# Kernel tuning notes

Measured on AMD Instinct MI355X. Metric: run time of the kernel, lower is better.

The kernel has to match this reference:

```python
import jax, jax.numpy as jnp
import numpy as np

N_NODES = 100000
N_EDGES = 1600000
C = 64            # in_channels == out_channels
EC = 32           # edge_channels


def setup_inputs() -> dict:
    key = jax.random.key(0)
    ks = jax.random.split(key, 8)
    s = 1.0 / np.sqrt(C)
    x = jax.random.normal(ks[0], (N_NODES, C), dtype=jnp.float32)
    edge_index = jax.random.randint(ks[1], (2, N_EDGES), 0, N_NODES, dtype=jnp.int64)
    edge_attr = jax.random.normal(ks[2], (N_EDGES, EC), dtype=jnp.float32)
    We = jax.random.uniform(ks[3], (C, EC), minval=-1/np.sqrt(EC), maxval=1/np.sqrt(EC), dtype=jnp.float32)  # edge_lin weight
    W = jax.random.uniform(ks[4], (C, C), minval=-s, maxval=s, dtype=jnp.float32)   # GatedGraphConv weight[0]
    W_ih = jax.random.uniform(ks[5], (3 * C, C), minval=-s, maxval=s, dtype=jnp.float32)
    W_hh = jax.random.uniform(ks[6], (3 * C, C), minval=-s, maxval=s, dtype=jnp.float32)
    b_ih = jnp.zeros((3 * C,), dtype=jnp.float32)
    b_hh = jnp.zeros((3 * C,), dtype=jnp.float32)
    return {"x": x, "edge_index": edge_index, "edge_attr": edge_attr,
            "We": We, "W": W, "W_ih": W_ih, "W_hh": W_hh, "b_ih": b_ih, "b_hh": b_hh}


def reference(x, edge_index, edge_attr, We, W, W_ih, W_hh, b_ih, b_hh):
    n_nodes = x.shape[0]
    # edge_lin: [E, EC] -> [E, C]
    ew = edge_attr @ We.T
    # GatedGraphConv, num_layers=1, aggr='add'
    m = x @ W                                  # [N, C]
    src, dst = edge_index[0], edge_index[1]
    msg = m[src] * ew                          # gather + elementwise edge weight, [E, C]
    agg = jax.ops.segment_sum(msg, dst, num_segments=n_nodes)  # scatter-add
    # GRUCell(agg, x)
    gi = agg @ W_ih.T + b_ih                   # [N, 3C]
    gh = x @ W_hh.T + b_hh                     # [N, 3C]
    i_r, i_z, i_n = jnp.split(gi, 3, axis=-1)
    h_r, h_z, h_n = jnp.split(gh, 3, axis=-1)
    r = jax.nn.sigmoid(i_r + h_r)
    z = jax.nn.sigmoid(i_z + h_z)
    n = jnp.tanh(i_n + r * h_n)
    h = (1.0 - z) * n + z * x
    out = jax.nn.relu(h)
    # residual blend, alpha = 0.5, res_lin = Identity (in == out channels)
    return 0.5 * out + 0.5 * x
```

## Files before the change

kernel.cpp:

```cpp
#include <hip/hip_runtime.h>
#include <math.h>

#define NN 100000
#define NE 1600000
#define CC 64
#define CAP 64

typedef unsigned int uint;
typedef _Float16 f16;
typedef _Float16 h2 __attribute__((ext_vector_type(2)));
typedef _Float16 f16x8 __attribute__((ext_vector_type(8)));
typedef float f32x4 __attribute__((ext_vector_type(4)));

__global__ __launch_bounds__(256) void k_xW(const float* __restrict__ x,
                                            const float* __restrict__ W,
                                            f16* __restrict__ mh,
                                            f16* __restrict__ xh) {
    __shared__ float xs[64][64];
    __shared__ float wsm[64][64];
    const int t = threadIdx.x;
    const int j = t & 63;
    const int g = t >> 6;
    const int base = blockIdx.x * 64;
    const int jperm = (j & 15) * 4 + (j >> 4);
#pragma unroll
    for (int r = 0; r < 16; ++r) {
        int idx = r * 256 + t;
        wsm[idx >> 6][idx & 63] = W[idx];
    }
#pragma unroll
    for (int r = 0; r < 16; ++r) {
        int idx = r * 256 + t;
        int n = idx >> 6, k = idx & 63;
        int gi = base + n;
        float v = 0.f;
        if (gi < NN) {
            v = x[(size_t)gi * 64 + k];
            xh[(size_t)gi * 64 + k] = (f16)v;
        }
        xs[n][k] = v;
    }
    __syncthreads();
    float acc[16];
#pragma unroll
    for (int q = 0; q < 16; ++q) acc[q] = 0.f;
    for (int k = 0; k < 64; ++k) {
        float w = wsm[k][j];
#pragma unroll
        for (int q = 0; q < 16; ++q)
            acc[q] = fmaf(xs[g * 16 + q][k], w, acc[q]);
    }
#pragma unroll
    for (int q = 0; q < 16; ++q) {
        int n = base + g * 16 + q;
        if (n < NN) mh[(size_t)n * 64 + jperm] = (f16)acc[q];
    }
}

__global__ __launch_bounds__(256) void k_pos2(const int* __restrict__ ei,
                                              int* __restrict__ cnt,
                                              int2* __restrict__ pe_pad) {
    int i = blockIdx.x * 256 + threadIdx.x;
    int stride = gridDim.x * 256;
    for (int e = i; e < NE; e += stride) {
        int d = ei[NE + e];
        int s = ei[e];
        int old = atomicAdd(&cnt[d], 1);
        if (old < CAP)
            pe_pad[(size_t)d * CAP + old] = make_int2(e, s);
    }
}

__global__ __launch_bounds__(256) void k_agg(const int* __restrict__ cnt,
                                             const int2* __restrict__ pe_pad,
                                             const float* __restrict__ ea,
                                             const f16* __restrict__ mh2,
                                             const float* __restrict__ We,
                                             f16* __restrict__ aggh) {
    const int t = threadIdx.x;
    const int lane = t & 63;
    const int wv = t >> 6;
    const int p = lane & 15;
    const int g = lane >> 4;
    f16x8 bf0, bf1, bf2, bf3;
    {
        const float* w0 = We + (0 * 16 + p) * 32 + g * 8;
        const float* w1 = We + (1 * 16 + p) * 32 + g * 8;
        const float* w2 = We + (2 * 16 + p) * 32 + g * 8;
        const float* w3 = We + (3 * 16 + p) * 32 + g * 8;
#pragma unroll
        for (int j = 0; j < 8; ++j) {
            bf0[j] = (f16)w0[j]; bf1[j] = (f16)w1[j];
            bf2[j] = (f16)w2[j]; bf3[j] = (f16)w3[j];
        }
    }
    const int wid = blockIdx.x * 4 + wv;
    const int nw = gridDim.x * 4;
    for (int n = wid; n < NN; n += nw) {
        int deg = cnt[n];
        deg = (deg > CAP) ? CAP : deg;
        const int2* bin = pe_pad + (size_t)n * CAP;
        float acc0 = 0.f, acc1 = 0.f, acc2 = 0.f, acc3 = 0.f;
        for (int s0 = 0; s0 < deg; s0 += 16) {
            int nb = deg - s0; nb = (nb > 16) ? 16 : nb;
            int2 v = bin[s0 + (p < nb ? p : 0)];
            const float4* rp = (const float4*)(ea + (size_t)v.x * 32 + g * 8);
            float4 q0 = rp[0];
            float4 q1 = rp[1];
            int srcv = v.y;
            f16x8 af;
            af[0] = (f16)q0.x; af[1] = (f16)q0.y;
            af[2] = (f16)q0.z; af[3] = (f16)q0.w;
            af[4] = (f16)q1.x; af[5] = (f16)q1.y;
            af[6] = (f16)q1.z; af[7] = (f16)q1.w;
            f32x4 c0 = {0.f, 0.f, 0.f, 0.f};
            f32x4 c1 = {0.f, 0.f, 0.f, 0.f};
            f32x4 c2 = {0.f, 0.f, 0.f, 0.f};
            f32x4 c3 = {0.f, 0.f, 0.f, 0.f};
            c0 = __builtin_amdgcn_mfma_f32_16x16x32_f16(af, bf0, c0, 0, 0, 0);
            c1 = __builtin_amdgcn_mfma_f32_16x16x32_f16(af, bf1, c1, 0, 0, 0);
            c2 = __builtin_amdgcn_mfma_f32_16x16x32_f16(af, bf2, c2, 0, 0, 0);
            c3 = __builtin_amdgcn_mfma_f32_16x16x32_f16(af, bf3, c3, 0, 0, 0);
#pragma unroll
            for (int r = 0; r < 4; ++r) {
                int er = g * 4 + r;
                int src = __shfl(srcv, er);
                uint2 md = *(const uint2*)(mh2 + (size_t)src * 64 + p * 4);
                h2 mlo = __builtin_bit_cast(h2, md.x);
                h2 mhi = __builtin_bit_cast(h2, md.y);
                float m0 = (float)mlo[0], m1 = (float)mlo[1];
                float m2 = (float)mhi[0], m3 = (float)mhi[1];
                if (er >= nb) { m0 = 0.f; m1 = 0.f; m2 = 0.f; m3 = 0.f; }
                acc0 = fmaf(c0[r], m0, acc0);
                acc1 = fmaf(c1[r], m1, acc1);
                acc2 = fmaf(c2[r], m2, acc2);
                acc3 = fmaf(c3[r], m3, acc3);
            }
        }
        acc0 += __shfl_xor(acc0, 16); acc0 += __shfl_xor(acc0, 32);
        acc1 += __shfl_xor(acc1, 16); acc1 += __shfl_xor(acc1, 32);
        acc2 += __shfl_xor(acc2, 16); acc2 += __shfl_xor(acc2, 32);
        acc3 += __shfl_xor(acc3, 16); acc3 += __shfl_xor(acc3, 32);
        float v = (g == 0) ? acc0 : (g == 1) ? acc1 : (g == 2) ? acc2 : acc3;
        aggh[(size_t)n * 64 + lane] = (f16)v;
    }
}

__global__ __launch_bounds__(256) void k_gru(const f16* __restrict__ aggh,
                                             const f16* __restrict__ xh,
                                             const float* __restrict__ Wih,
                                             const float* __restrict__ Whh,
                                             const float* __restrict__ bih,
                                             const float* __restrict__ bhh,
                                             float* __restrict__ out) {
    __shared__ f16 wl[192 * 136];
    const int t = threadIdx.x;
    const int lane = t & 63;
    const int wv = t >> 6;
    const int p = lane & 15;
    const int g = lane >> 4;
#pragma unroll
    for (int i = 0; i < 48; ++i) {
        int idx = i * 256 + t;
        int c = idx >> 6, k = idx & 63;
        wl[c * 136 + k] = (f16)Wih[idx];
        wl[c * 136 + 64 + k] = (f16)Whh[idx];
    }
    float bihv[12], bhhv[12];
#pragma unroll
    for (int i = 0; i < 12; ++i) {
        bihv[i] = bih[i * 16 + p];
        bhhv[i] = bhh[i * 16 + p];
    }
    __syncthreads();
    const int wid = blockIdx.x * 4 + wv;
    const int nw = gridDim.x * 4;
    for (int b = wid; b < NN / 16; b += nw) {
        const f16* ar = aggh + (size_t)b * 16 * 64;
        const f16* xr = xh + (size_t)b * 16 * 64;
        const int ro = p * 64 + g * 8;
        f16x8 a0 = *(const f16x8*)(ar + ro);
        f16x8 a1 = *(const f16x8*)(ar + ro + 32);
        f16x8 x0 = *(const f16x8*)(xr + ro);
        f16x8 x1 = *(const f16x8*)(xr + ro + 32);
#pragma unroll
        for (int nt = 0; nt < 4; ++nt) {
            const f16* w0 = wl + (nt * 16 + p) * 136 + g * 8;
            const f16* w1 = wl + ((nt + 4) * 16 + p) * 136 + g * 8;
            const f16* w2 = wl + ((nt + 8) * 16 + p) * 136 + g * 8;
            f32x4 cir = {0.f, 0.f, 0.f, 0.f};
            f32x4 ciz = {0.f, 0.f, 0.f, 0.f};
            f32x4 cin = {0.f, 0.f, 0.f, 0.f};
            f32x4 chr_ = {0.f, 0.f, 0.f, 0.f};
            f32x4 chz = {0.f, 0.f, 0.f, 0.f};
            f32x4 chn = {0.f, 0.f, 0.f, 0.f};
            cir = __builtin_amdgcn_mfma_f32_16x16x32_f16(a0, *(const f16x8*)(w0), cir, 0, 0, 0);
            cir = __builtin_amdgcn_mfma_f32_16x16x32_f16(a1, *(const f16x8*)(w0 + 32), cir, 0, 0, 0);
            ciz = __builtin_amdgcn_mfma_f32_16x16x32_f16(a0, *(const f16x8*)(w1), ciz, 0, 0, 0);
            ciz = __builtin_amdgcn_mfma_f32_16x16x32_f16(a1, *(const f16x8*)(w1 + 32), ciz, 0, 0, 0);
            cin = __builtin_amdgcn_mfma_f32_16x16x32_f16(a0, *(const f16x8*)(w2), cin, 0, 0, 0);
            cin = __builtin_amdgcn_mfma_f32_16x16x32_f16(a1, *(const f16x8*)(w2 + 32), cin, 0, 0, 0);
            chr_ = __builtin_amdgcn_mfma_f32_16x16x32_f16(x0, *(const f16x8*)(w0 + 64), chr_, 0, 0, 0);
            chr_ = __builtin_amdgcn_mfma_f32_16x16x32_f16(x1, *(const f16x8*)(w0 + 96), chr_, 0, 0, 0);
            chz = __builtin_amdgcn_mfma_f32_16x16x32_f16(x0, *(const f16x8*)(w1 + 64), chz, 0, 0, 0);
            chz = __builtin_amdgcn_mfma_f32_16x16x32_f16(x1, *(const f16x8*)(w1 + 96), chz, 0, 0, 0);
            chn = __builtin_amdgcn_mfma_f32_16x16x32_f16(x0, *(const f16x8*)(w2 + 64), chn, 0, 0, 0);
            chn = __builtin_amdgcn_mfma_f32_16x16x32_f16(x1, *(const f16x8*)(w2 + 96), chn, 0, 0, 0);
            int c = nt * 16 + p;
#pragma unroll
            for (int r4 = 0; r4 < 4; ++r4) {
                int node = b * 16 + g * 4 + r4;
                float pr = cir[r4] + bihv[nt] + chr_[r4] + bhhv[nt];
                float pz = ciz[r4] + bihv[nt + 4] + chz[r4] + bhhv[nt + 4];
                float tin = cin[r4] + bihv[nt + 8];
                float thn = chn[r4] + bhhv[nt + 8];
                float rr = 1.f / (1.f + __expf(-pr));
                float zz = 1.f / (1.f + __expf(-pz));
                float tt = tin + rr * thn;
                float nn = 2.f / (1.f + __expf(-2.f * tt)) - 1.f;
                float xv = (float)xh[(size_t)node * 64 + c];
                float h = (1.f - zz) * nn + zz * xv;
                float o = h > 0.f ? h : 0.f;
                out[(size_t)node * 64 + c] = 0.5f * o + 0.5f * xv;
            }
        }
    }
}

extern "C" void kernel_launch(void* const* d_in, const int* in_sizes, int n_in,
                              void* d_out, int out_size, void* d_ws, size_t ws_size,
                              hipStream_t stream) {
    const float* x   = (const float*)d_in[0];
    const int*   ei  = (const int*)d_in[1];
    const float* ea  = (const float*)d_in[2];
    const float* We  = (const float*)d_in[3];
    const float* W   = (const float*)d_in[4];
    const float* Wih = (const float*)d_in[5];
    const float* Whh = (const float*)d_in[6];
    const float* bih = (const float*)d_in[7];
    const float* bhh = (const float*)d_in[8];
    float* out = (float*)d_out;

    char* ws = (char*)d_ws;
    f16* mh = (f16*)ws;
    size_t off = ((size_t)NN * CC * 2 + 255) & ~(size_t)255;
    f16* xh   = (f16*)(ws + off); off += ((size_t)NN * CC * 2 + 255) & ~(size_t)255;
    f16* aggh = (f16*)(ws + off); off += ((size_t)NN * CC * 2 + 255) & ~(size_t)255;
    int2* pe_pad = (int2*)(ws + off); off += (size_t)NN * CAP * 8;
    int* cnt  = (int*)(ws + off); off += (size_t)NN * 4;

    (void)in_sizes; (void)n_in; (void)out_size; (void)ws_size;

    int nb_nodes = (NN + 63) / 64;
    k_xW<<<nb_nodes, 256, 0, stream>>>(x, W, mh, xh);
    hipMemsetAsync(cnt, 0, (size_t)NN * sizeof(int), stream);
    k_pos2<<<2048, 256, 0, stream>>>(ei, cnt, pe_pad);
    k_agg<<<4096, 256, 0, stream>>>(cnt, pe_pad, ea, mh, We, aggh);
    k_gru<<<768, 256, 0, stream>>>(aggh, xh, Wih, Whh, bih, bhh, out);
}
```

Before: 257.4 us.

## Fuse front kernels and pre-convert edge attributes to fp16 in a streaming pass

```diff
diff --git a/kernel.cpp b/kernel.cpp
--- a/kernel.cpp
+++ b/kernel.cpp
@@ -5,6 +5,8 @@
 #define NE 1600000
 #define CC 64
 #define CAP 64
+#define NBXW ((NN + 63) / 64)
+#define GFRONT 2048
 
 typedef unsigned int uint;
 typedef _Float16 f16;
@@ -12,68 +14,92 @@
 typedef _Float16 f16x8 __attribute__((ext_vector_type(8)));
 typedef float f32x4 __attribute__((ext_vector_type(4)));
 
-__global__ __launch_bounds__(256) void k_xW(const float* __restrict__ x,
-                                            const float* __restrict__ W,
-                                            f16* __restrict__ mh,
-                                            f16* __restrict__ xh) {
+__device__ __forceinline__ uint pk2(float a, float b) {
+    f16 x = (f16)a, y = (f16)b;
+    return (uint)__builtin_bit_cast(unsigned short, x) |
+           ((uint)__builtin_bit_cast(unsigned short, y) << 16);
+}
+
+__global__ __launch_bounds__(256) void k_front(const float* __restrict__ x,
+                                               const float* __restrict__ W,
+                                               const int* __restrict__ ei,
+                                               const float* __restrict__ ea,
+                                               f16* __restrict__ mh,
+                                               f16* __restrict__ xh,
+                                               uint4* __restrict__ eah4,
+                                               int* __restrict__ cnt,
+                                               int2* __restrict__ pe_pad) {
     __shared__ float xs[64][64];
     __shared__ float wsm[64][64];
+    const int b = blockIdx.x;
     const int t = threadIdx.x;
-    const int j = t & 63;
-    const int g = t >> 6;
-    const int base = blockIdx.x * 64;
-    const int jperm = (j & 15) * 4 + (j >> 4);
-#pragma unroll
-    for (int r = 0; r < 16; ++r) {
-        int idx = r * 256 + t;
-        wsm[idx >> 6][idx & 63] = W[idx];
-    }
-#pragma unroll
-    for (int r = 0; r < 16; ++r) {
-        int idx = r * 256 + t;
-        int n = idx >> 6, k = idx & 63;
-        int gi = base + n;
-        float v = 0.f;
-        if (gi < NN) {
-            v = x[(size_t)gi * 64 + k];
-            xh[(size_t)gi * 64 + k] = (f16)v;
-        }
-        xs[n][k] = v;
-    }
-    __syncthreads();
-    float acc[16];
-#pragma unroll
-    for (int q = 0; q < 16; ++q) acc[q] = 0.f;
-    for (int k = 0; k < 64; ++k) {
-        float w = wsm[k][j];
-#pragma unroll
-        for (int q = 0; q < 16; ++q)
-            acc[q] = fmaf(xs[g * 16 + q][k], w, acc[q]);
-    }
-#pragma unroll
-    for (int q = 0; q < 16; ++q) {
-        int n = base + g * 16 + q;
-        if (n < NN) mh[(size_t)n * 64 + jperm] = (f16)acc[q];
-    }
-}
-
-__global__ __launch_bounds__(256) void k_pos2(const int* __restrict__ ei,
-                                              int* __restrict__ cnt,
-                                              int2* __restrict__ pe_pad) {
-    int i = blockIdx.x * 256 + threadIdx.x;
-    int stride = gridDim.x * 256;
-    for (int e = i; e < NE; e += stride) {
-        int d = ei[NE + e];
-        int s = ei[e];
-        int old = atomicAdd(&cnt[d], 1);
-        if (old < CAP)
-            pe_pad[(size_t)d * CAP + old] = make_int2(e, s);
+
+    {
+        int i = b * 256 + t;
+        const int stride = GFRONT * 256;
+        for (int e = i; e < NE; e += stride) {
+            int d = ei[NE + e];
+            int s = ei[e];
+            int old = atomicAdd(&cnt[d], 1);
+            if (old < CAP)
+                pe_pad[(size_t)d * CAP + old] = make_int2(e, s);
+        }
+    }
+    {
+        const float4* ea4 = (const float4*)ea;
+        const int total = NE * 4;
+        int i = b * 256 + t;
+        const int stride = GFRONT * 256;
+        for (; i < total; i += stride) {
+            float4 a = ea4[2 * (size_t)i];
+            float4 c = ea4[2 * (size_t)i + 1];
+            eah4[i] = make_uint4(pk2(a.x, a.y), pk2(a.z, a.w),
+                                 pk2(c.x, c.y), pk2(c.z, c.w));
+        }
+    }
+    if (b < NBXW) {
+        const int j = t & 63;
+        const int g = t >> 6;
+        const int base = b * 64;
+        const int jperm = (j & 15) * 4 + (j >> 4);
+#pragma unroll
+        for (int r = 0; r < 16; ++r) {
+            int idx = r * 256 + t;
+            wsm[idx >> 6][idx & 63] = W[idx];
+        }
+#pragma unroll
+        for (int r = 0; r < 16; ++r) {
+            int idx = r * 256 + t;
+            int n = idx >> 6, k = idx & 63;
+            int gi = base + n;
+            float v = 0.f;
+            if (gi < NN) {
+                v = x[(size_t)gi * 64 + k];
+                xh[(size_t)gi * 64 + k] = (f16)v;
+            }
+            xs[n][k] = v;
+        }
+        __syncthreads();
+        float acc[16];
+#pragma unroll
+        for (int q = 0; q < 16; ++q) acc[q] = 0.f;
+        for (int k = 0; k < 64; ++k) {
+            float w = wsm[k][j];
+#pragma unroll
+            for (int q = 0; q < 16; ++q)
+                acc[q] = fmaf(xs[g * 16 + q][k], w, acc[q]);
+        }
+#pragma unroll
+        for (int q = 0; q < 16; ++q) {
+            int n = base + g * 16 + q;
+            if (n < NN) mh[(size_t)n * 64 + jperm] = (f16)acc[q];
+        }
     }
 }
 
 __global__ __launch_bounds__(256) void k_agg(const int* __restrict__ cnt,
                                              const int2* __restrict__ pe_pad,
-                                             const float* __restrict__ ea,
+                                             const f16* __restrict__ eah,
                                              const f16* __restrict__ mh2,
                                              const float* __restrict__ We,
                                              f16* __restrict__ aggh) {
@@ -104,15 +130,8 @@
         for (int s0 = 0; s0 < deg; s0 += 16) {
             int nb = deg - s0; nb = (nb > 16) ? 16 : nb;
             int2 v = bin[s0 + (p < nb ? p : 0)];
-            const float4* rp = (const float4*)(ea + (size_t)v.x * 32 + g * 8);
-            float4 q0 = rp[0];
-            float4 q1 = rp[1];
+            f16x8 af = *(const f16x8*)(eah + (size_t)v.x * 32 + g * 8);
             int srcv = v.y;
-            f16x8 af;
-            af[0] = (f16)q0.x; af[1] = (f16)q0.y;
-            af[2] = (f16)q0.z; af[3] = (f16)q0.w;
-            af[4] = (f16)q1.x; af[5] = (f16)q1.y;
-            af[6] = (f16)q1.z; af[7] = (f16)q1.w;
             f32x4 c0 = {0.f, 0.f, 0.f, 0.f};
             f32x4 c1 = {0.f, 0.f, 0.f, 0.f};
             f32x4 c2 = {0.f, 0.f, 0.f, 0.f};
@@ -246,15 +265,15 @@
     size_t off = ((size_t)NN * CC * 2 + 255) & ~(size_t)255;
     f16* xh   = (f16*)(ws + off); off += ((size_t)NN * CC * 2 + 255) & ~(size_t)255;
     f16* aggh = (f16*)(ws + off); off += ((size_t)NN * CC * 2 + 255) & ~(size_t)255;
+    f16* eah  = (f16*)(ws + off); off += (size_t)NE * 32 * 2;
     int2* pe_pad = (int2*)(ws + off); off += (size_t)NN * CAP * 8;
     int* cnt  = (int*)(ws + off); off += (size_t)NN * 4;
 
     (void)in_sizes; (void)n_in; (void)out_size; (void)ws_size;
 
-    int nb_nodes = (NN + 63) / 64;
-    k_xW<<<nb_nodes, 256, 0, stream>>>(x, W, mh, xh);
     hipMemsetAsync(cnt, 0, (size_t)NN * sizeof(int), stream);
-    k_pos2<<<2048, 256, 0, stream>>>(ei, cnt, pe_pad);
-    k_agg<<<4096, 256, 0, stream>>>(cnt, pe_pad, ea, mh, We, aggh);
+    k_front<<<GFRONT, 256, 0, stream>>>(x, W, ei, ea, mh, xh,
+                                        (uint4*)eah, cnt, pe_pad);
+    k_agg<<<4096, 256, 0, stream>>>(cnt, pe_pad, eah, mh, We, aggh);
     k_gru<<<768, 256, 0, stream>>>(aggh, xh, Wih, Whh, bih, bhh, out);
 }
```

Measured after the change: 297.4 us. 15.5% more time.
